# Performance work log

Hardware: AMD Instinct MI355X
Metric: run time of the kernel (lower is better)

The kernel has to match this reference:

```python
import jax, jax.numpy as jnp
import numpy as np

# Qwen3-Next-like dims
B, S, HID = 2, 2048, 2048
H, KV, D, ROT = 16, 2, 128, 32
G = H // KV              # kv repeat groups
SCALE = D ** -0.5
EPS = 1e-6
BETA_BIAS, BIAS_CAP = 1.0, 3.0   # L1 logit bias
BETA_POST = 0.5                  # L2 post-softmax rescale
ALPHA_K, ALPHA_V = 0.1, 0.1      # L4 k/v rescale
GMIN, GMAX = 0.9, 1.1
EMIN, EMAX = 0.9, 1.1


def setup_inputs() -> dict:
    key = jax.random.key(0)
    ks = jax.random.split(key, 10)
    hidden_states = jax.random.normal(ks[0], (B, S, HID), jnp.float32)
    # partial rotary embeddings (rot_dim = head_dim // 4)
    pos = jnp.arange(S, dtype=jnp.float32)
    inv = 1.0 / (10000.0 ** (jnp.arange(0, ROT, 2, dtype=jnp.float32) / ROT))
    freqs = pos[:, None] * inv[None, :]
    emb = jnp.concatenate([freqs, freqs], axis=-1)          # [S, ROT]
    cos = jnp.broadcast_to(jnp.cos(emb)[None], (B, S, ROT)).astype(jnp.float32)
    sin = jnp.broadcast_to(jnp.sin(emb)[None], (B, S, ROT)).astype(jnp.float32)
    # additive causal mask [B,1,S,S]
    causal = jnp.tril(jnp.ones((S, S), jnp.bool_))
    attention_mask = jnp.where(causal, 0.0, -1e9).astype(jnp.float32)
    attention_mask = jnp.broadcast_to(attention_mask[None, None], (B, 1, S, S))
    # key prior: positive, sums to 1 over kv_len
    prior = jax.nn.softmax(jax.random.normal(ks[1], (S,), jnp.float32))
    s = 0.02
    Wq = jax.random.normal(ks[2], (HID, H * D * 2), jnp.float32) * s
    Wk = jax.random.normal(ks[3], (HID, KV * D), jnp.float32) * s
    Wv = jax.random.normal(ks[4], (HID, KV * D), jnp.float32) * s
    Wo = jax.random.normal(ks[5], (H * D, HID), jnp.float32) * s
    q_norm_w = 1.0 + 0.02 * jax.random.normal(ks[6], (D,), jnp.float32)
    k_norm_w = 1.0 + 0.02 * jax.random.normal(ks[7], (D,), jnp.float32)
    return {"hidden_states": hidden_states, "cos": cos, "sin": sin,
            "attention_mask": attention_mask, "prior": prior,
            "Wq": Wq, "Wk": Wk, "Wv": Wv, "Wo": Wo,
            "q_norm_w": q_norm_w, "k_norm_w": k_norm_w}


def _rms(x, w):
    return x * jax.lax.rsqrt(jnp.mean(x * x, axis=-1, keepdims=True) + EPS) * w


def _rot_half(x):
    x1, x2 = jnp.split(x, 2, axis=-1)
    return jnp.concatenate([-x2, x1], axis=-1)


def _rope(x, cos, sin):
    # x: [B,h,S,D]; rotary on first ROT dims only (Qwen3-Next partial rotary)
    xr, xp = x[..., :ROT], x[..., ROT:]
    xr = xr * cos + _rot_half(xr) * sin
    return jnp.concatenate([xr, xp], axis=-1)


def reference(hidden_states, cos, sin, attention_mask, prior, Wq, Wk, Wv, Wo, q_norm_w, k_norm_w):
    h = hidden_states
    # gated q projection: chunk into query + gate
    qg = (h @ Wq).reshape(B, S, H, 2 * D)
    q, gate = qg[..., :D], qg[..., D:]
    gate = gate.reshape(B, S, H * D)
    q = _rms(q, q_norm_w).transpose(0, 2, 1, 3)                       # [B,H,S,D]
    k = _rms((h @ Wk).reshape(B, S, KV, D), k_norm_w).transpose(0, 2, 1, 3)  # [B,KV,S,D]
    v = (h @ Wv).reshape(B, S, KV, D).transpose(0, 2, 1, 3)
    c, s_ = cos[:, None], sin[:, None]                                # [B,1,S,ROT]
    q, k = _rope(q, c, s_), _rope(k, c, s_)
    k = jnp.repeat(k, G, axis=1)                                      # GQA expand -> [B,H,S,D]
    v = jnp.repeat(v, G, axis=1)
    # L4: prior-based elementwise k/v rescale with clamped gamma/eta
    pc = prior * S                                                    # mean ~1 over keys
    gamma = jnp.clip(1.0 + ALPHA_K * (pc - 1.0), GMIN, GMAX)
    eta = jnp.clip(1.0 + ALPHA_V * (pc - 1.0), EMIN, EMAX)
    k = k * gamma[None, None, :, None]
    v = v * eta[None, None, :, None]
    scores = jnp.einsum('bhqd,bhkd->bhqk', q, k) * SCALE
    # L1: capped steering bias on logits
    scores = scores + jnp.clip(BETA_BIAS * prior, -BIAS_CAP, BIAS_CAP)[None, None, None, :]
    scores = scores + attention_mask
    probs = jax.nn.softmax(scores.astype(jnp.float32), axis=-1)       # fp32 softmax
    # L2: post-softmax prior rescale + renorm
    p2 = probs * (1.0 + BETA_POST * pc)[None, None, None, :]
    probs = p2 / jnp.sum(p2, axis=-1, keepdims=True)
    out = jnp.einsum('bhqk,bhkd->bhqd', probs.astype(h.dtype), v)
    out = out.transpose(0, 2, 1, 3).reshape(B, S, H * D)
    out = out * jax.nn.sigmoid(gate)                                  # gated attention output
    return out @ Wo
```

## Files before the change

### kernel.cpp

```cpp
#include <hip/hip_runtime.h>
#include <hip/hip_bf16.h>
#include <stdint.h>

#define B_    2
#define S_    2048
#define HID_  2048
#define H_    16
#define KV_   2
#define D_    128
#define ROT_  32
#define QGS   4608
#define SCALE_ 0.08838834764831845f

typedef __attribute__((ext_vector_type(8))) short  short8;
typedef __attribute__((ext_vector_type(4))) float  floatx4;

__device__ __forceinline__ float b2f(unsigned short u) {
  union { unsigned int i; float f; } v; v.i = ((unsigned int)u) << 16; return v.f;
}
__device__ __forceinline__ unsigned short f2b(float f) {
  union { float f; unsigned int i; } v; v.f = f;
  return (unsigned short)((v.i + 0x7fffu + ((v.i >> 16) & 1u)) >> 16);
}
__device__ __forceinline__ void gload_lds16(const unsigned short* g, unsigned short* l) {
  __builtin_amdgcn_global_load_lds((const __attribute__((address_space(1))) void*)g,
                                   (__attribute__((address_space(3))) void*)l, 16, 0, 0);
}

__device__ __forceinline__ void transpose_body(const float* __restrict__ in,
                                               unsigned short* __restrict__ out,
                                               int R, int C, int bx, int by, int t) {
  __shared__ unsigned short tile[64][68];
  int tx = t & 15, ty = t >> 4;
  long c0 = (long)bx * 64, r0 = (long)by * 64;
#pragma unroll
  for (int i = 0; i < 4; i++) {
    int row = ty + 16 * i;
    const float* src = in + (r0 + row) * C + c0 + 4 * tx;
    float4 v = *(const float4*)src;
    tile[row][4 * tx + 0] = f2b(v.x);
    tile[row][4 * tx + 1] = f2b(v.y);
    tile[row][4 * tx + 2] = f2b(v.z);
    tile[row][4 * tx + 3] = f2b(v.w);
  }
  __syncthreads();
#pragma unroll
  for (int i = 0; i < 4; i++) {
    int oc = ty + 16 * i;
    ushort4 v;
    v.x = tile[4 * tx + 0][oc];
    v.y = tile[4 * tx + 1][oc];
    v.z = tile[4 * tx + 2][oc];
    v.w = tile[4 * tx + 3][oc];
    *(ushort4*)(out + (c0 + oc) * R + r0 + 4 * tx) = v;
  }
}

__global__ __launch_bounds__(256) void k_preproc(const float* __restrict__ h_f,
                                                 const float* __restrict__ prior,
                                                 const float* __restrict__ Wq,
                                                 const float* __restrict__ Wk,
                                                 const float* __restrict__ Wv,
                                                 const float* __restrict__ Wo,
                                                 unsigned short* __restrict__ hb,
                                                 unsigned short* __restrict__ WqkvT,
                                                 unsigned short* __restrict__ WoT,
                                                 float* __restrict__ ge,
                                                 float* __restrict__ kbias) {
  int bx = blockIdx.x;
  const int t = threadIdx.x;
  if (bx < 8) {
    int i = bx * 256 + t;
    float p  = prior[i];
    float pc = p * (float)S_;
    float g  = 1.0f + 0.1f * (pc - 1.0f);
    g = fminf(fmaxf(g, 0.9f), 1.1f);
    ge[i] = g;
    float cb = fminf(fmaxf(p, -3.0f), 3.0f);
    kbias[i] = cb + logf(1.0f + 0.5f * pc);
    return;
  }
  bx -= 8;
  if (bx < 4096) {
    long i0 = ((long)bx * 256 + t) * 8;
    float4 a = *(const float4*)(h_f + i0);
    float4 b = *(const float4*)(h_f + i0 + 4);
    short8 v;
    v[0] = (short)f2b(a.x); v[1] = (short)f2b(a.y);
    v[2] = (short)f2b(a.z); v[3] = (short)f2b(a.w);
    v[4] = (short)f2b(b.x); v[5] = (short)f2b(b.y);
    v[6] = (short)f2b(b.z); v[7] = (short)f2b(b.w);
    *(short8*)(hb + i0) = v;
    return;
  }
  bx -= 4096;
  if (bx < 2048) { transpose_body(Wq, WqkvT, 2048, 4096, bx & 63, bx >> 6, t); return; }
  bx -= 2048;
  if (bx < 1024) { transpose_body(Wo, WoT, 2048, 2048, bx & 31, bx >> 5, t); return; }
  bx -= 1024;
  if (bx < 128)  { transpose_body(Wk, WqkvT + (size_t)4096 * 2048, 2048, 256, bx & 3, bx >> 2, t); return; }
  bx -= 128;
  transpose_body(Wv, WqkvT + (size_t)4352 * 2048, 2048, 256, bx & 3, bx >> 2, t);
}

template <int OUT32>
__global__ __launch_bounds__(256) void k_gemm_bt(const unsigned short* __restrict__ A,
                                                 const unsigned short* __restrict__ Bt,
                                                 void* __restrict__ Cv,
                                                 int M, int N, int K) {
  __shared__ __align__(16) unsigned short As[2][128 * 32];
  __shared__ __align__(16) unsigned short Bs[2][128 * 32];
  const int t    = threadIdx.x;
  const int lane = t & 63;
  const int wv   = t >> 6;
  const int wm   = wv >> 1, wn = wv & 1;
  const long m0  = (long)blockIdx.y * 128;
  const long n0  = (long)blockIdx.x * 128;
  const int r15  = lane & 15, g4 = lane >> 4;

  const int srow = lane >> 2;
  const int scol = ((lane & 3) ^ ((lane >> 3) & 3)) * 8;
  const unsigned short* sA0 = A  + (m0 + wv * 16 + srow)       * K + scol;
  const unsigned short* sA1 = A  + (m0 + (wv + 4) * 16 + srow) * K + scol;
  const unsigned short* sB0 = Bt + (n0 + wv * 16 + srow)       * K + scol;
  const unsigned short* sB1 = Bt + (n0 + (wv + 4) * 16 + srow) * K + scol;

  floatx4 acc[4][4];
#pragma unroll
  for (int m = 0; m < 4; m++)
#pragma unroll
    for (int n = 0; n < 4; n++) acc[m][n] = (floatx4){0.f, 0.f, 0.f, 0.f};

  gload_lds16(sA0, &As[0][wv * 512]);
  gload_lds16(sA1, &As[0][(wv + 4) * 512]);
  gload_lds16(sB0, &Bs[0][wv * 512]);
  gload_lds16(sB1, &Bs[0][(wv + 4) * 512]);
  __syncthreads();

  const int fcol = (g4 ^ ((r15 >> 1) & 3)) * 8;
  int cur = 0;
  for (int k0 = 0; k0 < K; k0 += 32) {
    if (k0 + 32 < K) {
      const int nx = cur ^ 1, ko = k0 + 32;
      gload_lds16(sA0 + ko, &As[nx][wv * 512]);
      gload_lds16(sA1 + ko, &As[nx][(wv + 4) * 512]);
      gload_lds16(sB0 + ko, &Bs[nx][wv * 512]);
      gload_lds16(sB1 + ko, &Bs[nx][(wv + 4) * 512]);
    }
    short8 af[4], bf[4];
#pragma unroll
    for (int m = 0; m < 4; m++)
      af[m] = *(const short8*)(&As[cur][(wm * 64 + m * 16 + r15) * 32 + fcol]);
#pragma unroll
    for (int n = 0; n < 4; n++)
      bf[n] = *(const short8*)(&Bs[cur][(wn * 64 + n * 16 + r15) * 32 + fcol]);
#pragma unroll
    for (int m = 0; m < 4; m++)
#pragma unroll
      for (int n = 0; n < 4; n++)
        acc[m][n] = __builtin_amdgcn_mfma_f32_16x16x32_bf16(af[m], bf[n], acc[m][n], 0, 0, 0);
    __syncthreads();
    cur ^= 1;
  }

#pragma unroll
  for (int m = 0; m < 4; m++) {
    const long rbase = m0 + wm * 64 + m * 16 + g4 * 4;
#pragma unroll
    for (int n = 0; n < 4; n++) {
      const long cidx = n0 + wn * 64 + n * 16 + r15;
#pragma unroll
      for (int i = 0; i < 4; i++) {
        if (OUT32) ((float*)Cv)[(rbase + i) * N + cidx] = acc[m][n][i];
        else ((unsigned short*)Cv)[(rbase + i) * N + cidx] = f2b(acc[m][n][i]);
      }
    }
  }
}

__global__ __launch_bounds__(256) void k_qkvpost(const unsigned short* __restrict__ qgkv,
                                                 const float* __restrict__ cosb,
                                                 const float* __restrict__ sinb,
                                                 const float* __restrict__ ge,
                                                 const float* __restrict__ qnw,
                                                 const float* __restrict__ knw,
                                                 unsigned short* __restrict__ qT,
                                                 unsigned short* __restrict__ kF,
                                                 unsigned short* __restrict__ vF) {
  int bxx = blockIdx.x;
  if (bxx < 18432) {
    int wid  = (bxx * 256 + (int)threadIdx.x) >> 6;
    int lane = threadIdx.x & 63;
    int r    = wid % (H_ + KV_);
    long bs  = wid / (H_ + KV_);
    int b = (int)(bs >> 11), s = (int)(bs & 2047);
    int d0 = lane * 2;

    float x0, x1;
    if (r < H_) {
      const unsigned short* src = qgkv + bs * QGS + r * 256 + d0;
      x0 = b2f(src[0]); x1 = b2f(src[1]);
    } else {
      const unsigned short* src = qgkv + bs * QGS + 4096 + (r - H_) * 128 + d0;
      x0 = b2f(src[0]); x1 = b2f(src[1]);
    }
    float ss = x0 * x0 + x1 * x1;
#pragma unroll
    for (int mask = 1; mask < 64; mask <<= 1) ss += __shfl_xor(ss, mask);
    float rstd = rsqrtf(ss * (1.0f / 128.0f) + 1e-6f);
    float w0, w1;
    if (r < H_) { w0 = qnw[d0]; w1 = qnw[d0 + 1]; }
    else        { w0 = knw[d0]; w1 = knw[d0 + 1]; }
    float xn0 = x0 * rstd * w0, xn1 = x1 * rstd * w1;
    float p0 = __shfl_xor(xn0, 8), p1 = __shfl_xor(xn1, 8);
    float y0 = xn0, y1 = xn1;
    if (lane < 16) {
      float c0 = cosb[bs * ROT_ + d0], c1 = cosb[bs * ROT_ + d0 + 1];
      float s0 = sinb[bs * ROT_ + d0], s1 = sinb[bs * ROT_ + d0 + 1];
      float sgn = (lane < 8) ? -1.0f : 1.0f;
      y0 = xn0 * c0 + sgn * p0 * s0;
      y1 = xn1 * c1 + sgn * p1 * s1;
    }
    if (r < H_) {
      unsigned int pack = (unsigned int)f2b(y0) | ((unsigned int)f2b(y1) << 16);
      *(unsigned int*)(qT + ((long)(b * H_ + r) * S_ + s) * D_ + d0) = pack;
    } else {
      float g = ge[s];
      unsigned int pack = (unsigned int)f2b(y0 * g) | ((unsigned int)f2b(y1 * g) << 16);
      int kvb = r - H_;
      size_t off = (size_t)(b * KV_ + kvb) * 262144
                 + (size_t)((s >> 4) * 4 + (d0 >> 5)) * 512
                 + (size_t)(((s & 15) + (((d0 >> 3) & 3)) * 16)) * 8 + (d0 & 7);
      *(unsigned int*)(kF + off) = pack;
    }
  } else {
    int bx  = bxx - 18432;
    int scn = bx & 7, d = (bx >> 3) & 127, kvb = (bx >> 10) & 1, b = bx >> 11;
    int s = scn * 256 + threadIdx.x;
    float v = b2f(qgkv[((long)(b * S_ + s)) * QGS + 4352 + kvb * 128 + d]);
    v *= ge[s];
    size_t off = (size_t)(b * KV_ + kvb) * 262144
               + (size_t)((s >> 6) * 16 + (d >> 4) * 2 + ((s >> 5) & 1)) * 512
               + (size_t)((d & 15) + ((s >> 3) & 3) * 16) * 8 + (s & 7);
    vF[off] = f2b(v);
  }
}

__global__ __launch_bounds__(256) void k_attn(const unsigned short* __restrict__ qT,
                                              const unsigned short* __restrict__ kF,
                                              const unsigned short* __restrict__ vF,
                                              const float* __restrict__ kbias,
                                              const unsigned short* __restrict__ qgkv,
                                              unsigned short* __restrict__ ag) {
  __shared__ __align__(16) unsigned short KL[2][8192];
  __shared__ __align__(16) unsigned short Ps[4][16 * 88];
  const int t = threadIdx.x;
  const int lane = t & 63, wv = t >> 6;
  const int r15 = lane & 15, g4 = lane >> 4;
  const int p = blockIdx.x;
  const int xcd = p & 7;
  const int grp = xcd >> 1;
  const int mem = ((p >> 3) << 1) | (xcd & 1);
  const int head = mem & 7;
  const int quad = 31 - (mem >> 3);
  const int b = grp >> 1, kvh = grp & 1;
  const int hh = kvh * 8 + head;
  const int strip = quad * 4 + wv;
  const int q0s = strip * 16;
  const int ntiles = quad + 1;

  const unsigned short* kFg = kF + (size_t)(b * KV_ + kvh) * 262144;
  const unsigned short* vFg = vF + (size_t)(b * KV_ + kvh) * 262144;

  short8 qf[4];
  {
    const unsigned short* qp = qT + ((long)(b * H_ + hh) * S_ + q0s + r15) * D_ + g4 * 8;
#pragma unroll
    for (int kb = 0; kb < 4; kb++) qf[kb] = *(const short8*)(qp + kb * 32);
  }

  floatx4 oacc[8];
#pragma unroll
  for (int nd = 0; nd < 8; nd++) oacc[nd] = (floatx4){0.f, 0.f, 0.f, 0.f};
  float mrow = -1e30f, lrw = 0.f;

#pragma unroll
  for (int i = 0; i < 4; i++)
    gload_lds16(kFg + (size_t)wv * 2048 + i * 512 + lane * 8, &KL[0][wv * 2048 + i * 512]);
  __syncthreads();

  int cur = 0;
  for (int tile = 0; tile < ntiles; tile++) {
    if (tile + 1 < ntiles) {
      const size_t src = (size_t)(tile + 1) * 8192 + wv * 2048 + lane * 8;
#pragma unroll
      for (int i = 0; i < 4; i++)
        gload_lds16(kFg + src + i * 512, &KL[cur ^ 1][wv * 2048 + i * 512]);
    }

    floatx4 sacc[4];
#pragma unroll
    for (int n = 0; n < 4; n++) sacc[n] = (floatx4){0.f, 0.f, 0.f, 0.f};
    __builtin_amdgcn_s_setprio(1);
#pragma unroll
    for (int n = 0; n < 4; n++) {
      const unsigned short* kl = &KL[cur][n * 2048 + lane * 8];
      short8 a0 = *(const short8*)(kl);
      short8 a1 = *(const short8*)(kl + 512);
      short8 a2 = *(const short8*)(kl + 1024);
      short8 a3 = *(const short8*)(kl + 1536);
      sacc[n] = __builtin_amdgcn_mfma_f32_16x16x32_bf16(a0, qf[0], sacc[n], 0, 0, 0);
      sacc[n] = __builtin_amdgcn_mfma_f32_16x16x32_bf16(a1, qf[1], sacc[n], 0, 0, 0);
      sacc[n] = __builtin_amdgcn_mfma_f32_16x16x32_bf16(a2, qf[2], sacc[n], 0, 0, 0);
      sacc[n] = __builtin_amdgcn_mfma_f32_16x16x32_bf16(a3, qf[3], sacc[n], 0, 0, 0);
    }
    __builtin_amdgcn_s_setprio(0);

    const unsigned short* vt = vFg + (size_t)tile * 8192 + lane * 8;
    short8 vfA[8];
#pragma unroll
    for (int nd = 0; nd < 8; nd++) vfA[nd] = *(const short8*)(vt + (nd * 2) * 512);

    const bool last = (tile == ntiles - 1);
    float scf[4][4];
#pragma unroll
    for (int n = 0; n < 4; n++) {
      const int j0 = tile * 64;
      float4 kb4 = *(const float4*)(&kbias[j0 + n * 16 + g4 * 4]);
#pragma unroll
      for (int i = 0; i < 4; i++) {
        float kbv = (i == 0) ? kb4.x : (i == 1) ? kb4.y : (i == 2) ? kb4.z : kb4.w;
        float v = sacc[n][i] * SCALE_ + kbv;
        if (last) {
          int jg = j0 + n * 16 + g4 * 4 + i;
          if (jg > q0s + r15) v = -1e30f;
        }
        scf[n][i] = v;
      }
    }
    float pmax = scf[0][0];
#pragma unroll
    for (int n = 0; n < 4; n++)
#pragma unroll
      for (int i = 0; i < 4; i++) pmax = fmaxf(pmax, scf[n][i]);
    pmax = fmaxf(pmax, __shfl_xor(pmax, 16));
    pmax = fmaxf(pmax, __shfl_xor(pmax, 32));
    if (__any(pmax > mrow + 8.0f)) {
      float mn = fmaxf(mrow, pmax);
      float aq = __expf(mrow - mn);
      mrow = mn;
      lrw *= aq;
      float ai[4];
#pragma unroll
      for (int i = 0; i < 4; i++) ai[i] = __shfl(aq, g4 * 4 + i);
#pragma unroll
      for (int nd = 0; nd < 8; nd++)
#pragma unroll
        for (int i = 0; i < 4; i++) oacc[nd][i] *= ai[i];
    }
    float rsum = 0.f;
#pragma unroll
    for (int n = 0; n < 4; n++)
#pragma unroll
      for (int i = 0; i < 4; i++) {
        float pv = __expf(scf[n][i] - mrow);
        scf[n][i] = pv;
        rsum += pv;
      }
    rsum += __shfl_xor(rsum, 16);
    rsum += __shfl_xor(rsum, 32);
    lrw += rsum;

#pragma unroll
    for (int n = 0; n < 4; n++) {
      unsigned int lo = (unsigned int)f2b(scf[n][0]) | ((unsigned int)f2b(scf[n][1]) << 16);
      unsigned int hi = (unsigned int)f2b(scf[n][2]) | ((unsigned int)f2b(scf[n][3]) << 16);
      uint2 w; w.x = lo; w.y = hi;
      *(uint2*)(&Ps[wv][r15 * 88 + n * 16 + g4 * 4]) = w;
    }

    short8 vfB[8];
#pragma unroll
    for (int nd = 0; nd < 8; nd++) vfB[nd] = *(const short8*)(vt + (nd * 2 + 1) * 512);

    {
      __builtin_amdgcn_s_setprio(1);
      short8 pa0 = *(const short8*)(&Ps[wv][r15 * 88 + g4 * 8]);
#pragma unroll
      for (int nd = 0; nd < 8; nd++)
        oacc[nd] = __builtin_amdgcn_mfma_f32_16x16x32_bf16(pa0, vfA[nd], oacc[nd], 0, 0, 0);
      short8 pa1 = *(const short8*)(&Ps[wv][r15 * 88 + 32 + g4 * 8]);
#pragma unroll
      for (int nd = 0; nd < 8; nd++)
        oacc[nd] = __builtin_amdgcn_mfma_f32_16x16x32_bf16(pa1, vfB[nd], oacc[nd], 0, 0, 0);
      __builtin_amdgcn_s_setprio(0);
    }
    __syncthreads();
    cur ^= 1;
  }

  float il[4];
#pragma unroll
  for (int i = 0; i < 4; i++) il[i] = __shfl(lrw, g4 * 4 + i);
#pragma unroll
  for (int i = 0; i < 4; i++) {
    int q = q0s + g4 * 4 + i;
    float inv = 1.0f / il[i];
    const unsigned short* gptr = qgkv + ((size_t)(b * S_ + q)) * QGS + hh * 256 + 128;
    unsigned short* aptr = ag + ((size_t)(b * S_ + q)) * (H_ * D_) + hh * D_;
#pragma unroll
    for (int nd = 0; nd < 8; nd++) {
      int d = nd * 16 + r15;
      float gt = b2f(gptr[d]);
      float sg = 1.0f / (1.0f + __expf(-gt));
      aptr[d] = f2b(oacc[nd][i] * inv * sg);
    }
  }
}

extern "C" void kernel_launch(void* const* d_in, const int* in_sizes, int n_in,
                              void* d_out, int out_size, void* d_ws, size_t ws_size,
                              hipStream_t stream) {
  const float* h_f   = (const float*)d_in[0];
  const float* cosb  = (const float*)d_in[1];
  const float* sinb  = (const float*)d_in[2];
  const float* prior = (const float*)d_in[4];
  const float* Wq    = (const float*)d_in[5];
  const float* Wk    = (const float*)d_in[6];
  const float* Wv    = (const float*)d_in[7];
  const float* Wo    = (const float*)d_in[8];
  const float* qnw   = (const float*)d_in[9];
  const float* knw   = (const float*)d_in[10];

  char* ws = (char*)d_ws;
  size_t off = 0;
  auto alloc = [&](size_t bytes) { char* p = ws + off; off += (bytes + 255) & ~(size_t)255; return p; };
  unsigned short* hb    = (unsigned short*)alloc((size_t)4096 * 2048 * 2);
  unsigned short* WqkvT = (unsigned short*)alloc((size_t)4608 * 2048 * 2);
  unsigned short* WoT   = (unsigned short*)alloc((size_t)2048 * 2048 * 2);
  unsigned short* qgkv  = (unsigned short*)alloc((size_t)4096 * QGS * 2);
  unsigned short* qTb   = (unsigned short*)alloc((size_t)B_ * H_ * S_ * D_ * 2);
  unsigned short* kF    = (unsigned short*)alloc((size_t)B_ * KV_ * S_ * D_ * 2);
  unsigned short* vF    = (unsigned short*)alloc((size_t)B_ * KV_ * S_ * D_ * 2);
  float* ge    = (float*)alloc((size_t)S_ * 4);
  float* kbias = (float*)alloc((size_t)S_ * 4);
  unsigned short* ag = hb;

  dim3 blk(256);
  k_preproc<<<dim3(7432), blk, 0, stream>>>(h_f, prior, Wq, Wk, Wv, Wo,
                                            hb, WqkvT, WoT, ge, kbias);
  k_gemm_bt<0><<<dim3(36, 32), blk, 0, stream>>>(hb, WqkvT, qgkv, 4096, QGS, 2048);
  k_qkvpost<<<dim3(22528), blk, 0, stream>>>(qgkv, cosb, sinb, ge, qnw, knw, qTb, kF, vF);
  k_attn<<<dim3(1024), blk, 0, stream>>>(qTb, kF, vF, kbias, qgkv, ag);
  k_gemm_bt<1><<<dim3(16, 32), blk, 0, stream>>>(ag, WoT, d_out, 4096, 2048, 2048);
}
```

Measured before the change: 269.4 us.

## Fuse Q RMSNorm and RoPE into attention prologue; remap GEMM blocks across XCDs

Moves the per-head Q RMSNorm and partial rotary embedding out of the post-GEMM kernel and into the attention kernel's Q fragment load, which now reads raw q straight from the projection output. This drops the qT intermediate buffer and its write and re-read, and shrinks the post-processing launch to K and V work only. The GEMM kernel also remaps its block indices so consecutive tiles are spread across the eight XCDs, aiming for better L2 locality. The risk is a slightly longer attention prologue and strided 16-byte Q reads from the wide qgkv rows.

```diff
diff --git a/kernel.cpp b/kernel.cpp
--- a/kernel.cpp
+++ b/kernel.cpp
@@ -114,8 +114,12 @@
   const int lane = t & 63;
   const int wv   = t >> 6;
   const int wm   = wv >> 1, wn = wv & 1;
-  const long m0  = (long)blockIdx.y * 128;
-  const long n0  = (long)blockIdx.x * 128;
+  const int nwg  = gridDim.x * gridDim.y;
+  const int orig = blockIdx.y * gridDim.x + blockIdx.x;
+  const int wg   = (orig & 7) * (nwg >> 3) + (orig >> 3);
+  const int bxx  = wg % gridDim.x, byy = wg / gridDim.x;
+  const long m0  = (long)byy * 128;
+  const long n0  = (long)bxx * 128;
   const int r15  = lane & 15, g4 = lane >> 4;
 
   const int srow = lane >> 2;
@@ -182,35 +186,25 @@
                                                  const float* __restrict__ cosb,
                                                  const float* __restrict__ sinb,
                                                  const float* __restrict__ ge,
-                                                 const float* __restrict__ qnw,
                                                  const float* __restrict__ knw,
-                                                 unsigned short* __restrict__ qT,
                                                  unsigned short* __restrict__ kF,
                                                  unsigned short* __restrict__ vF) {
   int bxx = blockIdx.x;
-  if (bxx < 18432) {
-    int wid  = (bxx * 256 + (int)threadIdx.x) >> 6;
+  if (bxx < 2048) {
+    int wid  = bxx * 4 + ((int)threadIdx.x >> 6);
     int lane = threadIdx.x & 63;
-    int r    = wid % (H_ + KV_);
-    long bs  = wid / (H_ + KV_);
+    int kvb  = wid & 1;
+    long bs  = wid >> 1;
     int b = (int)(bs >> 11), s = (int)(bs & 2047);
     int d0 = lane * 2;
 
-    float x0, x1;
-    if (r < H_) {
-      const unsigned short* src = qgkv + bs * QGS + r * 256 + d0;
-      x0 = b2f(src[0]); x1 = b2f(src[1]);
-    } else {
-      const unsigned short* src = qgkv + bs * QGS + 4096 + (r - H_) * 128 + d0;
-      x0 = b2f(src[0]); x1 = b2f(src[1]);
-    }
+    const unsigned short* src = qgkv + bs * QGS + 4096 + kvb * 128 + d0;
+    float x0 = b2f(src[0]), x1 = b2f(src[1]);
     float ss = x0 * x0 + x1 * x1;
 #pragma unroll
     for (int mask = 1; mask < 64; mask <<= 1) ss += __shfl_xor(ss, mask);
     float rstd = rsqrtf(ss * (1.0f / 128.0f) + 1e-6f);
-    float w0, w1;
-    if (r < H_) { w0 = qnw[d0]; w1 = qnw[d0 + 1]; }
-    else        { w0 = knw[d0]; w1 = knw[d0 + 1]; }
+    float w0 = knw[d0], w1 = knw[d0 + 1];
     float xn0 = x0 * rstd * w0, xn1 = x1 * rstd * w1;
     float p0 = __shfl_xor(xn0, 8), p1 = __shfl_xor(xn1, 8);
     float y0 = xn0, y1 = xn1;
@@ -221,20 +215,14 @@
       y0 = xn0 * c0 + sgn * p0 * s0;
       y1 = xn1 * c1 + sgn * p1 * s1;
     }
-    if (r < H_) {
-      unsigned int pack = (unsigned int)f2b(y0) | ((unsigned int)f2b(y1) << 16);
-      *(unsigned int*)(qT + ((long)(b * H_ + r) * S_ + s) * D_ + d0) = pack;
-    } else {
-      float g = ge[s];
-      unsigned int pack = (unsigned int)f2b(y0 * g) | ((unsigned int)f2b(y1 * g) << 16);
-      int kvb = r - H_;
-      size_t off = (size_t)(b * KV_ + kvb) * 262144
-                 + (size_t)((s >> 4) * 4 + (d0 >> 5)) * 512
-                 + (size_t)(((s & 15) + (((d0 >> 3) & 3)) * 16)) * 8 + (d0 & 7);
-      *(unsigned int*)(kF + off) = pack;
-    }
+    float g = ge[s];
+    unsigned int pack = (unsigned int)f2b(y0 * g) | ((unsigned int)f2b(y1 * g) << 16);
+    size_t off = (size_t)(b * KV_ + kvb) * 262144
+               + (size_t)((s >> 4) * 4 + (d0 >> 5)) * 512
+               + (size_t)(((s & 15) + (((d0 >> 3) & 3)) * 16)) * 8 + (d0 & 7);
+    *(unsigned int*)(kF + off) = pack;
   } else {
-    int bx  = bxx - 18432;
+    int bx  = bxx - 2048;
     int scn = bx & 7, d = (bx >> 3) & 127, kvb = (bx >> 10) & 1, b = bx >> 11;
     int s = scn * 256 + threadIdx.x;
     float v = b2f(qgkv[((long)(b * S_ + s)) * QGS + 4352 + kvb * 128 + d]);
@@ -246,11 +234,13 @@
   }
 }
 
-__global__ __launch_bounds__(256) void k_attn(const unsigned short* __restrict__ qT,
+__global__ __launch_bounds__(256) void k_attn(const unsigned short* __restrict__ qgkv,
                                               const unsigned short* __restrict__ kF,
                                               const unsigned short* __restrict__ vF,
                                               const float* __restrict__ kbias,
-                                              const unsigned short* __restrict__ qgkv,
+                                              const float* __restrict__ cosb,
+                                              const float* __restrict__ sinb,
+                                              const float* __restrict__ qnw,
                                               unsigned short* __restrict__ ag) {
   __shared__ __align__(16) unsigned short KL[2][8192];
   __shared__ __align__(16) unsigned short Ps[4][16 * 88];
@@ -274,9 +264,50 @@
 
   short8 qf[4];
   {
-    const unsigned short* qp = qT + ((long)(b * H_ + hh) * S_ + q0s + r15) * D_ + g4 * 8;
-#pragma unroll
-    for (int kb = 0; kb < 4; kb++) qf[kb] = *(const short8*)(qp + kb * 32);
+    const int q = q0s + r15;
+    const unsigned short* qp = qgkv + ((size_t)(b * S_) + q) * QGS + hh * 256 + g4 * 8;
+    float xn[4][8];
+    float ssq = 0.f;
+#pragma unroll
+    for (int kb = 0; kb < 4; kb++) {
+      short8 qr = *(const short8*)(qp + kb * 32);
+#pragma unroll
+      for (int e = 0; e < 8; e++) {
+        float x = b2f((unsigned short)qr[e]);
+        xn[kb][e] = x;
+        ssq += x * x;
+      }
+    }
+    ssq += __shfl_xor(ssq, 16);
+    ssq += __shfl_xor(ssq, 32);
+    float rstd = rsqrtf(ssq * (1.0f / 128.0f) + 1e-6f);
+#pragma unroll
+    for (int kb = 0; kb < 4; kb++) {
+      float4 w0 = *(const float4*)(&qnw[kb * 32 + g4 * 8]);
+      float4 w1 = *(const float4*)(&qnw[kb * 32 + g4 * 8 + 4]);
+      xn[kb][0] *= rstd * w0.x; xn[kb][1] *= rstd * w0.y;
+      xn[kb][2] *= rstd * w0.z; xn[kb][3] *= rstd * w0.w;
+      xn[kb][4] *= rstd * w1.x; xn[kb][5] *= rstd * w1.y;
+      xn[kb][6] *= rstd * w1.z; xn[kb][7] *= rstd * w1.w;
+    }
+    {
+      const float* cb = cosb + ((size_t)(b * S_) + q) * ROT_ + g4 * 8;
+      const float* sb = sinb + ((size_t)(b * S_) + q) * ROT_ + g4 * 8;
+      float4 c0 = *(const float4*)(cb), c1 = *(const float4*)(cb + 4);
+      float4 s0 = *(const float4*)(sb), s1 = *(const float4*)(sb + 4);
+      float cv[8] = {c0.x, c0.y, c0.z, c0.w, c1.x, c1.y, c1.z, c1.w};
+      float sv[8] = {s0.x, s0.y, s0.z, s0.w, s1.x, s1.y, s1.z, s1.w};
+      float sgn = (g4 < 2) ? -1.0f : 1.0f;
+#pragma unroll
+      for (int e = 0; e < 8; e++) {
+        float part = __shfl_xor(xn[0][e], 32);
+        xn[0][e] = xn[0][e] * cv[e] + sgn * part * sv[e];
+      }
+    }
+#pragma unroll
+    for (int kb = 0; kb < 4; kb++)
+#pragma unroll
+      for (int e = 0; e < 8; e++) qf[kb][e] = (short)f2b(xn[kb][e]);
   }
 
   floatx4 oacc[8];
@@ -439,7 +470,6 @@
   unsigned short* WqkvT = (unsigned short*)alloc((size_t)4608 * 2048 * 2);
   unsigned short* WoT   = (unsigned short*)alloc((size_t)2048 * 2048 * 2);
   unsigned short* qgkv  = (unsigned short*)alloc((size_t)4096 * QGS * 2);
-  unsigned short* qTb   = (unsigned short*)alloc((size_t)B_ * H_ * S_ * D_ * 2);
   unsigned short* kF    = (unsigned short*)alloc((size_t)B_ * KV_ * S_ * D_ * 2);
   unsigned short* vF    = (unsigned short*)alloc((size_t)B_ * KV_ * S_ * D_ * 2);
   float* ge    = (float*)alloc((size_t)S_ * 4);
@@ -450,7 +480,7 @@
   k_preproc<<<dim3(7432), blk, 0, stream>>>(h_f, prior, Wq, Wk, Wv, Wo,
                                             hb, WqkvT, WoT, ge, kbias);
   k_gemm_bt<0><<<dim3(36, 32), blk, 0, stream>>>(hb, WqkvT, qgkv, 4096, QGS, 2048);
-  k_qkvpost<<<dim3(22528), blk, 0, stream>>>(qgkv, cosb, sinb, ge, qnw, knw, qTb, kF, vF);
-  k_attn<<<dim3(1024), blk, 0, stream>>>(qTb, kF, vF, kbias, qgkv, ag);
+  k_qkvpost<<<dim3(6144), blk, 0, stream>>>(qgkv, cosb, sinb, ge, knw, kF, vF);
+  k_attn<<<dim3(1024), blk, 0, stream>>>(qgkv, kF, vF, kbias, cosb, sinb, qnw, ag);
   k_gemm_bt<1><<<dim3(16, 32), blk, 0, stream>>>(ag, WoT, d_out, 4096, 2048, 2048);
 }
```

New measurement: 268.6 us. Within noise of the previous version (-0.3%).
